# Kernel optimization log

Hardware: AMD Instinct MI355X
Metric: run time of the kernel (lower is better)

The kernel has to match this reference:

```python
import jax, jax.numpy as jnp
import numpy as np

B, S, CTX, DIM = 2, 2048, 2048, 2048
H, HKV, HD = 16, 4, 128
HID = 5464  # 4*ceil(int(4*DIM*2/3)/4)
EPS = 1.1920929e-07  # torch eps=None -> finfo(fp32).eps
REP = H // HKV


def rmsnorm(x, w):
    return x * jax.lax.rsqrt(jnp.mean(x * x, axis=-1, keepdims=True) + EPS) * w


def rotate_half(x):
    # interleaved rotate: out[::2] = -x[1::2], out[1::2] = x[::2]
    x2 = x.reshape(x.shape[:-1] + (-1, 2))
    return jnp.stack([-x2[..., 1], x2[..., 0]], axis=-1).reshape(x.shape)


def masked_attn(q, k, v, mask):
    # q,k,v: [B,H,Sq/Sk,D]; mask broadcastable to [B,H,Sq,Sk]
    scale = 1.0 / jnp.sqrt(jnp.asarray(q.shape[-1], q.dtype))
    s = jnp.einsum('bhqd,bhkd->bhqk', q, k) * scale
    s = jnp.where(mask, s, jnp.asarray(-1e30, s.dtype))
    p = jax.nn.softmax(s, axis=-1)
    p = jnp.where(mask, p, 0.0)  # fully-masked rows -> 0 output (flex_attention semantics)
    return jnp.einsum('bhqk,bhkd->bhqd', p, v)


def setup_inputs() -> dict:
    key = jax.random.key(0)
    ks = jax.random.split(key, 20)
    std = 0.02
    return {
        'x': jax.random.normal(ks[0], (B, S, DIM), jnp.float32),
        'context': jax.random.normal(ks[1], (B, CTX, DIM), jnp.float32),
        'freqs_cos': jax.random.uniform(ks[2], (S, 1, HD), jnp.float32),
        'freqs_sin': jax.random.uniform(ks[3], (S, 1, HD), jnp.float32),
        'wqkv': jax.random.normal(ks[4], ((H + 2 * HKV) * HD, DIM), jnp.float32) * std,
        'wo_self': jax.random.normal(ks[5], (DIM, DIM), jnp.float32) * std,
        'qn_self': jnp.ones((HD,), jnp.float32),
        'kn_self': jnp.ones((HD,), jnp.float32),
        'wq': jax.random.normal(ks[6], (H * HD, DIM), jnp.float32) * std,
        'wkv': jax.random.normal(ks[7], (2 * HKV * HD, DIM), jnp.float32) * std,
        'wo_cross': jax.random.normal(ks[8], (DIM, DIM), jnp.float32) * std,
        'qn_cross': jnp.ones((HD,), jnp.float32),
        'kn_cross': jnp.ones((HD,), jnp.float32),
        'w1': jax.random.normal(ks[9], (HID, DIM), jnp.float32) * std,
        'w2': jax.random.normal(ks[10], (DIM, HID), jnp.float32) * std,
        'attn_norm_w': jnp.ones((DIM,), jnp.float32),
        'cross_norm_w': jnp.ones((DIM,), jnp.float32),
        'ffn_norm_w': jnp.ones((DIM,), jnp.float32),
        'vis_mask': jax.random.randint(ks[11], (B, S), 0, 2).astype(bool),
        'context_mask': jax.random.randint(ks[12], (B, CTX), 0, 2).astype(bool),
    }


def reference(x, context, freqs_cos, freqs_sin, wqkv, wo_self, qn_self, kn_self,
              wq, wkv, wo_cross, qn_cross, kn_cross, w1, w2,
              attn_norm_w, cross_norm_w, ffn_norm_w, vis_mask, context_mask):
    b, s, _ = x.shape
    ctx = context.shape[1]

    # ---- self-attention (prenorm) ----
    h0 = rmsnorm(x, attn_norm_w)
    qkv = h0 @ wqkv.T
    xq = qkv[..., :H * HD].reshape(b, s, H, HD)
    xk = qkv[..., H * HD:(H + HKV) * HD].reshape(b, s, HKV, HD)
    xv = qkv[..., (H + HKV) * HD:].reshape(b, s, HKV, HD)
    xq = rmsnorm(xq, qn_self)   # qk-norm BEFORE rope in self-attn
    xk = rmsnorm(xk, kn_self)
    xq = xq * freqs_cos + rotate_half(xq) * freqs_sin
    xk = xk * freqs_cos + rotate_half(xk) * freqs_sin
    q = xq.transpose(0, 2, 1, 3)
    k = jnp.repeat(xk.transpose(0, 2, 1, 3), REP, axis=1)
    v = jnp.repeat(xv.transpose(0, 2, 1, 3), REP, axis=1)
    m_self = vis_mask[:, None, :, None] & vis_mask[:, None, None, :]
    a = masked_attn(q, k, v, m_self)
    h = x + a.transpose(0, 2, 1, 3).reshape(b, s, DIM) @ wo_self.T

    # ---- cross-attention (prenorm) ----
    hc = rmsnorm(h, cross_norm_w)
    xq = (hc @ wq.T).reshape(b, s, H, HD)
    kv = context @ wkv.T
    xk = kv[..., :HKV * HD].reshape(b, ctx, HKV, HD)
    xv = kv[..., HKV * HD:].reshape(b, ctx, HKV, HD)
    xq = xq * freqs_cos + rotate_half(xq) * freqs_sin  # rope on q BEFORE qk-norm in cross-attn
    xq = rmsnorm(xq, qn_cross)
    xk = rmsnorm(xk, kn_cross)
    q = xq.transpose(0, 2, 1, 3)
    k = jnp.repeat(xk.transpose(0, 2, 1, 3), REP, axis=1)
    v = jnp.repeat(xv.transpose(0, 2, 1, 3), REP, axis=1)
    m_cross = context_mask[:, None, None, :]
    a = masked_attn(q, k, v, m_cross)
    h = h + a.transpose(0, 2, 1, 3).reshape(b, s, DIM) @ wo_cross.T

    # ---- FFN (silu) ----
    hf = rmsnorm(h, ffn_norm_w)
    return h + jax.nn.silu(hf @ w1.T) @ w2.T
```

## Files before the change

### kernel.cpp

```cpp
#include <hip/hip_runtime.h>

#define DEVI __device__ __forceinline__

typedef __attribute__((ext_vector_type(4))) float f32x4;
typedef __attribute__((ext_vector_type(8))) __bf16 bf16x8;

static constexpr float EPS = 1.1920929e-07f;

DEVI float bf2f(unsigned short u){ return __uint_as_float(((unsigned)u)<<16); }
DEVI unsigned short f2bfu(float f){
  unsigned u = __float_as_uint(f);
  u += 0x7fffu + ((u>>16)&1u);
  return (unsigned short)(u>>16);
}
DEVI unsigned pack2(float a, float b){ return (unsigned)f2bfu(a) | ((unsigned)f2bfu(b)<<16); }

DEVI void gload16(const void* g, const void* l){
  __builtin_amdgcn_global_load_lds((const __attribute__((address_space(1))) void*)g,
                                   (__attribute__((address_space(3))) void*)l, 16, 0, 0);
}

__global__ void k_masknorm(const unsigned* __restrict__ vin, const unsigned* __restrict__ cin,
                           unsigned char* __restrict__ vout, unsigned char* __restrict__ cout){
  __shared__ int smode;
  const int t = threadIdx.x;
  if (t==0) smode = 0;
  __syncthreads();
  unsigned loc = 0;
  for (int i=t; i<1024; i+=256) loc |= (vin[i] > 1u);
  if (loc) smode = 1;
  __syncthreads();
  if (smode){
    for (int i=t; i<1024; i+=256){
      ((unsigned*)vout)[i] = vin[i];
      ((unsigned*)cout)[i] = cin[i];
    }
  } else {
    const int* vi = (const int*)vin; const int* ci = (const int*)cin;
    for (int i=t; i<4096; i+=256){
      vout[i] = (unsigned char)(vi[i] != 0);
      cout[i] = (unsigned char)(ci[i] != 0);
    }
  }
}

__global__ void k_conv(const float* __restrict__ s, unsigned short* __restrict__ d, int n4){
  int i = blockIdx.x*256 + threadIdx.x;
  if (i >= n4) return;
  float4 v = ((const float4*)s)[i];
  uint2 u; u.x = pack2(v.x, v.y); u.y = pack2(v.z, v.w);
  ((uint2*)d)[i] = u;
}
__global__ void k_convpad_rows(const float* __restrict__ s, unsigned short* __restrict__ d,
                               int R, int C, int Rp){
  int i = blockIdx.x*256 + threadIdx.x;
  int total = (Rp*C)>>2;
  if (i >= total) return;
  uint2 u; u.x = 0u; u.y = 0u;
  if (i*4 < R*C){ float4 v = ((const float4*)s)[i]; u.x = pack2(v.x,v.y); u.y = pack2(v.z,v.w); }
  ((uint2*)d)[i] = u;
}
__global__ void k_convpad_cols(const float* __restrict__ s, unsigned short* __restrict__ d,
                               int N, int K, int Kp){
  int i = blockIdx.x*256 + threadIdx.x;
  int total = (N*Kp)>>2;
  if (i >= total) return;
  int i4 = i*4; int n = i4/Kp; int k = i4 - n*Kp;
  uint2 u; u.x = 0u; u.y = 0u;
  if (k < K){ float4 v = *(const float4*)(s + (size_t)n*K + k); u.x = pack2(v.x,v.y); u.y = pack2(v.z,v.w); }
  ((uint2*)d)[i] = u;
}

__global__ void k_rms(const float* __restrict__ X, const float* __restrict__ W,
                      unsigned short* __restrict__ Y){
  const int row = blockIdx.x, tid = threadIdx.x;
  const float* x = X + (size_t)row*2048;
  float4 v0 = ((const float4*)x)[tid*2];
  float4 v1 = ((const float4*)x)[tid*2+1];
  float ss = v0.x*v0.x+v0.y*v0.y+v0.z*v0.z+v0.w*v0.w
           + v1.x*v1.x+v1.y*v1.y+v1.z*v1.z+v1.w*v1.w;
  #pragma unroll
  for (int o=32;o;o>>=1) ss += __shfl_xor(ss, o);
  __shared__ float red[4];
  if ((tid&63)==0) red[tid>>6] = ss;
  __syncthreads();
  float tot = red[0]+red[1]+red[2]+red[3];
  float rs = rsqrtf(tot*(1.0f/2048.0f) + EPS);
  float4 w0 = ((const float4*)W)[tid*2];
  float4 w1 = ((const float4*)W)[tid*2+1];
  uint4 u;
  u.x = pack2(v0.x*rs*w0.x, v0.y*rs*w0.y);
  u.y = pack2(v0.z*rs*w0.z, v0.w*rs*w0.w);
  u.z = pack2(v1.x*rs*w1.x, v1.y*rs*w1.y);
  u.w = pack2(v1.z*rs*w1.z, v1.w*rs*w1.w);
  *(uint4*)(Y + (size_t)row*2048 + tid*8) = u;
}

template<int EPI>
__global__ void k_gemm(const unsigned short* __restrict__ A, const unsigned short* __restrict__ Bw,
                       void* Cout, const float* resid, int M, int N, int K){
  __shared__ __align__(16) unsigned short sm[16384];
  const int tid = threadIdx.x;
  const int w = tid>>6, l = tid&63, g = l>>4, q = l&15;
  const int bm = blockIdx.y<<7, bn = blockIdx.x<<7;
  const int wr = (w>>1)<<6, wc = (w&1)<<6;
  f32x4 acc[4][4];
  #pragma unroll
  for (int a=0;a<4;++a)
    #pragma unroll
    for (int b2=0;b2<4;++b2) acc[a][b2] = f32x4{0.f,0.f,0.f,0.f};

  const unsigned short* Ag = A + (size_t)bm*K;
  const unsigned short* Bg = Bw + (size_t)bn*K;
  const int nk = K>>5;
  int cur = 0;

  auto STAGE = [&](int buf, int kt){
    #pragma unroll
    for (int i=0;i<2;++i){
      int L = (i*256+tid)*16;
      int r = L>>6; int ce = (L&63)>>1;
      int lofs = __builtin_amdgcn_readfirstlane(buf*8192 + i*4096 + (tid>>6)*1024);
      gload16(Ag + (size_t)r*K + (kt<<5) + ce, (const char*)sm + lofs);
    }
    #pragma unroll
    for (int i=0;i<2;++i){
      int L = (i*256+tid)*16;
      int r = L>>6; int ce = (L&63)>>1;
      int lofs = __builtin_amdgcn_readfirstlane(16384 + buf*8192 + i*4096 + (tid>>6)*1024);
      gload16(Bg + (size_t)r*K + (kt<<5) + ce, (const char*)sm + lofs);
    }
  };

  STAGE(0, 0);
  __syncthreads();
  for (int kt=0; kt<nk; ++kt){
    if (kt+1 < nk) STAGE(cur^1, kt+1);
    const unsigned short* Ab = sm + cur*4096;
    const unsigned short* Bb = sm + 8192 + cur*4096;
    bf16x8 af[4], bfr[4];
    #pragma unroll
    for (int mi=0;mi<4;++mi) af[mi] = *(const bf16x8*)(Ab + (wr + mi*16 + q)*32 + g*8);
    #pragma unroll
    for (int ni=0;ni<4;++ni) bfr[ni] = *(const bf16x8*)(Bb + (wc + ni*16 + q)*32 + g*8);
    #pragma unroll
    for (int mi=0;mi<4;++mi)
      #pragma unroll
      for (int ni=0;ni<4;++ni)
        acc[mi][ni] = __builtin_amdgcn_mfma_f32_16x16x32_bf16(af[mi], bfr[ni], acc[mi][ni], 0,0,0);
    __syncthreads();
    cur ^= 1;
  }
  #pragma unroll
  for (int mi=0;mi<4;++mi)
    #pragma unroll
    for (int ni=0;ni<4;++ni)
      #pragma unroll
      for (int r=0;r<4;++r){
        int row = bm + wr + mi*16 + g*4 + r;
        int col = bn + wc + ni*16 + q;
        size_t idx = (size_t)row*N + col;
        float v = acc[mi][ni][r];
        if (EPI==0) ((unsigned short*)Cout)[idx] = f2bfu(v);
        else if (EPI==1){ float sg = v/(1.0f+__expf(-v)); ((unsigned short*)Cout)[idx] = f2bfu(sg); }
        else ((float*)Cout)[idx] = resid[idx] + v;
      }
}

__global__ void k_self_pp(const unsigned short* __restrict__ qkv, const float* __restrict__ fc,
                          const float* __restrict__ fs, const float* __restrict__ qn,
                          const float* __restrict__ kn,
                          unsigned short* __restrict__ Qb, unsigned short* __restrict__ Kb,
                          unsigned short* __restrict__ Vt){
  const int row = blockIdx.x;
  const int b = row>>11, s = row&2047;
  const int w = threadIdx.x>>6, l = threadIdx.x&63;
  const int d0 = 2*l, d1 = d0+1;
  const float c0 = fc[s*128+d0], c1 = fc[s*128+d1];
  const float s0 = fs[s*128+d0], s1 = fs[s*128+d1];
  #pragma unroll
  for (int it=0; it<6; ++it){
    const int hh = it*4 + w;
    const unsigned short* src = qkv + (size_t)row*3072 + hh*128;
    if (hh >= 20){
      const int hv = hh - 20;
      size_t base = ((size_t)(b*4 + hv))*128*2048;
      Vt[base + (size_t)d0*2048 + s] = src[d0];
      Vt[base + (size_t)d1*2048 + s] = src[d1];
    } else {
      float x0 = bf2f(src[d0]), x1 = bf2f(src[d1]);
      float ss = x0*x0 + x1*x1;
      #pragma unroll
      for (int o=32;o;o>>=1) ss += __shfl_xor(ss, o);
      float rs = rsqrtf(ss*(1.0f/128.0f) + EPS);
      if (hh < 16){
        float y0 = x0*rs*qn[d0], y1 = x1*rs*qn[d1];
        *(unsigned*)(Qb + (((size_t)(b*16 + hh)*2048 + s)*128) + d0)
          = pack2(y0*c0 - y1*s0, y1*c1 + y0*s1);
      } else {
        float y0 = x0*rs*kn[d0], y1 = x1*rs*kn[d1];
        *(unsigned*)(Kb + (((size_t)(b*4 + (hh-16))*2048 + s)*128) + d0)
          = pack2(y0*c0 - y1*s0, y1*c1 + y0*s1);
      }
    }
  }
}

__global__ void k_crossq_pp(const unsigned short* __restrict__ qc, const float* __restrict__ fc,
                            const float* __restrict__ fs, const float* __restrict__ qn,
                            unsigned short* __restrict__ Qb){
  const int row = blockIdx.x;
  const int b = row>>11, s = row&2047;
  const int w = threadIdx.x>>6, l = threadIdx.x&63;
  const int d0 = 2*l, d1 = d0+1;
  const float c0 = fc[s*128+d0], c1 = fc[s*128+d1];
  const float s0 = fs[s*128+d0], s1 = fs[s*128+d1];
  #pragma unroll
  for (int it=0; it<4; ++it){
    const int hh = it*4 + w;
    const unsigned short* src = qc + (size_t)row*2048 + hh*128;
    float x0 = bf2f(src[d0]), x1 = bf2f(src[d1]);
    float y0 = x0*c0 - x1*s0;
    float y1 = x1*c1 + x0*s1;
    float ss = y0*y0 + y1*y1;
    #pragma unroll
    for (int o=32;o;o>>=1) ss += __shfl_xor(ss, o);
    float rs = rsqrtf(ss*(1.0f/128.0f) + EPS);
    *(unsigned*)(Qb + (((size_t)(b*16 + hh)*2048 + s)*128) + d0)
      = pack2(y0*rs*qn[d0], y1*rs*qn[d1]);
  }
}

__global__ void k_crosskv_pp(const unsigned short* __restrict__ kvc, const float* __restrict__ kn,
                             unsigned short* __restrict__ Kb, unsigned short* __restrict__ Vt){
  const int row = blockIdx.x;
  const int b = row>>11, s = row&2047;
  const int w = threadIdx.x>>6, l = threadIdx.x&63;
  const int d0 = 2*l, d1 = d0+1;
  #pragma unroll
  for (int it=0; it<2; ++it){
    const int hh = it*4 + w;
    const unsigned short* src = kvc + (size_t)row*1024 + hh*128;
    if (hh < 4){
      float x0 = bf2f(src[d0]), x1 = bf2f(src[d1]);
      float ss = x0*x0 + x1*x1;
      #pragma unroll
      for (int o=32;o;o>>=1) ss += __shfl_xor(ss, o);
      float rs = rsqrtf(ss*(1.0f/128.0f) + EPS);
      *(unsigned*)(Kb + (((size_t)(b*4 + hh)*2048 + s)*128) + d0)
        = pack2(x0*rs*kn[d0], x1*rs*kn[d1]);
    } else {
      const int hv = hh-4;
      size_t base = ((size_t)(b*4 + hv))*128*2048;
      Vt[base + (size_t)d0*2048 + s] = src[d0];
      Vt[base + (size_t)d1*2048 + s] = src[d1];
    }
  }
}

template<bool QMASK>
__global__ void k_attn(const unsigned short* __restrict__ Qg, const unsigned short* __restrict__ Kg,
                       const unsigned short* __restrict__ Vtg,
                       const unsigned char* __restrict__ qm, const unsigned char* __restrict__ km,
                       unsigned short* __restrict__ Og, int H, int HKV){
  constexpr int SK = 2048, SQ = 2048, NT = SK/64;
  constexpr float SCALE = 0.08838834764831845f;
  __shared__ __align__(16) char smem[75776];
  const int qt = blockIdx.x, h = blockIdx.y, b = blockIdx.z;
  const int hk = h / (H/HKV);
  const int tid = threadIdx.x, w = tid>>6, l = tid&63, g = l>>4, q = l&15;

  {
    const unsigned long long* mp = (const unsigned long long*)(km + (size_t)b*SK);
    ((unsigned long long*)(smem + 73728))[tid] = mp[tid];
  }

  const size_t qrow = (size_t)(b*H + h)*SQ + qt*64 + w*16 + q;
  bf16x8 qf[4];
  #pragma unroll
  for (int ks=0;ks<4;++ks) qf[ks] = *(const bf16x8*)(Qg + qrow*128 + ks*32 + g*8);

  f32x4 oacc[8];
  #pragma unroll
  for (int i=0;i<8;++i) oacc[i] = f32x4{0.f,0.f,0.f,0.f};
  float m_run = -1e30f, l_run = 0.f;

  const unsigned short* Kt0 = Kg + (size_t)(b*HKV + hk)*SK*128;
  const unsigned short* Vt0 = Vtg + (size_t)(b*HKV + hk)*128*SK;
  const unsigned char* mlds = (const unsigned char*)(smem + 73728);
  char* Pl = smem + 65536 + w*2048;

  auto STAGE_T = [&](int t, int p){
    #pragma unroll
    for (int i=0;i<4;++i){
      int L = (i*256+tid)*16;
      int r = L>>8, c16 = (L>>4)&15;
      int c = (c16 & 8) | ((c16 & 7) ^ (r & 7));
      int lofs = __builtin_amdgcn_readfirstlane(p*16384 + i*4096 + w*1024);
      gload16(Kt0 + (size_t)(t*64 + r)*128 + c*8, smem + lofs);
    }
    #pragma unroll
    for (int i=0;i<4;++i){
      int L = (i*256+tid)*16;
      int d = L>>7, c8 = (L>>4)&7;
      int c = c8 ^ (d & 7);
      int lofs = __builtin_amdgcn_readfirstlane(32768 + p*16384 + i*4096 + w*1024);
      gload16(Vt0 + (size_t)d*SK + t*64 + c*8, smem + lofs);
    }
  };

  STAGE_T(0, 0);

  for (int t=0; t<NT; ++t){
    const int p = t&1;
    asm volatile("s_waitcnt lgkmcnt(0)" ::: "memory");
    __builtin_amdgcn_s_barrier();
    asm volatile("" ::: "memory");
    if (t+1 < NT){
      STAGE_T(t+1, p^1);
      asm volatile("s_waitcnt vmcnt(8)" ::: "memory");
    } else {
      asm volatile("s_waitcnt vmcnt(0)" ::: "memory");
    }
    __builtin_amdgcn_s_barrier();
    asm volatile("" ::: "memory");

    const char* Kb_ = smem + p*16384;
    const char* Vb_ = smem + 32768 + p*16384;

    f32x4 sacc[4];
    #pragma unroll
    for (int i=0;i<4;++i) sacc[i] = f32x4{0.f,0.f,0.f,0.f};
    __builtin_amdgcn_s_setprio(1);
    #pragma unroll
    for (int ks=0;ks<4;++ks){
      #pragma unroll
      for (int mi=0;mi<4;++mi){
        int kcol = mi*16 + q;
        int c = 4*ks + g;
        int c16 = (c & 8) | ((c & 7) ^ (kcol & 7));
        bf16x8 ak = *(const bf16x8*)(Kb_ + kcol*256 + c16*16);
        sacc[mi] = __builtin_amdgcn_mfma_f32_16x16x32_bf16(ak, qf[ks], sacc[mi], 0,0,0);
      }
    }
    __builtin_amdgcn_s_setprio(0);
    float sv[4][4];
    float mloc = -1e30f;
    #pragma unroll
    for (int mi=0;mi<4;++mi)
      #pragma unroll
      for (int r=0;r<4;++r){
        int kidx = t*64 + mi*16 + g*4 + r;
        float v = mlds[kidx] ? sacc[mi][r]*SCALE : -1e30f;
        sv[mi][r] = v;
        mloc = fmaxf(mloc, v);
      }
    mloc = fmaxf(mloc, __shfl_xor(mloc, 16));
    mloc = fmaxf(mloc, __shfl_xor(mloc, 32));
    float mnew = fmaxf(m_run, mloc);
    float alpha = __expf(m_run - mnew);
    float rsum = 0.f;
    unsigned pb[4][2];
    #pragma unroll
    for (int mi=0;mi<4;++mi){
      float p0 = (sv[mi][0] > -5e29f) ? __expf(sv[mi][0] - mnew) : 0.f;
      float p1 = (sv[mi][1] > -5e29f) ? __expf(sv[mi][1] - mnew) : 0.f;
      float p2 = (sv[mi][2] > -5e29f) ? __expf(sv[mi][2] - mnew) : 0.f;
      float p3 = (sv[mi][3] > -5e29f) ? __expf(sv[mi][3] - mnew) : 0.f;
      float q0 = bf2f(f2bfu(p0)), q1 = bf2f(f2bfu(p1));
      float q2 = bf2f(f2bfu(p2)), q3 = bf2f(f2bfu(p3));
      rsum += (q0+q1)+(q2+q3);
      pb[mi][0] = pack2(q0, q1);
      pb[mi][1] = pack2(q2, q3);
    }
    rsum += __shfl_xor(rsum, 16);
    rsum += __shfl_xor(rsum, 32);
    l_run = l_run*alpha + rsum;
    m_run = mnew;
    #pragma unroll
    for (int i=0;i<8;++i) oacc[i] *= alpha;

    #pragma unroll
    for (int mi=0;mi<4;++mi){
      int c16 = (2*mi + (g>>1)) ^ (q & 7);
      uint2 uu; uu.x = pb[mi][0]; uu.y = pb[mi][1];
      *(uint2*)(Pl + q*128 + c16*16 + (g&1)*8) = uu;
    }
    asm volatile("" ::: "memory");

    __builtin_amdgcn_s_setprio(1);
    #pragma unroll
    for (int ks=0;ks<2;++ks){
      int c16 = (4*ks + g) ^ (q & 7);
      bf16x8 pf = *(const bf16x8*)(Pl + q*128 + c16*16);
      #pragma unroll
      for (int mi=0;mi<8;++mi){
        int d = mi*16 + q;
        bf16x8 vf = *(const bf16x8*)(Vb_ + d*128 + c16*16);
        oacc[mi] = __builtin_amdgcn_mfma_f32_16x16x32_bf16(vf, pf, oacc[mi], 0,0,0);
      }
    }
    __builtin_amdgcn_s_setprio(0);
  }

  float inv = (l_run > 0.f) ? 1.0f/l_run : 0.f;
  if (QMASK){
    if (!qm[(size_t)b*SQ + qt*64 + w*16 + q]) inv = 0.f;
  }
  __syncthreads();
  float* Ot = (float*)smem;
  #pragma unroll
  for (int mi=0;mi<8;++mi)
    #pragma unroll
    for (int r=0;r<4;++r){
      int d = mi*16 + g*4 + r;
      Ot[d*65 + w*16 + q] = oacc[mi][r]*inv;
    }
  __syncthreads();
  int qloc = tid>>2, seg = tid&3;
  int srow = qt*64 + qloc;
  size_t obase = ((size_t)b*SQ + srow)*(size_t)(H*128) + (size_t)h*128 + seg*32;
  #pragma unroll
  for (int p4=0;p4<4;++p4){
    float vv[8];
    #pragma unroll
    for (int j=0;j<8;++j) vv[j] = Ot[(seg*32 + p4*8 + j)*65 + qloc];
    uint4 u;
    u.x = pack2(vv[0],vv[1]); u.y = pack2(vv[2],vv[3]);
    u.z = pack2(vv[4],vv[5]); u.w = pack2(vv[6],vv[7]);
    *(uint4*)(Og + obase + p4*8) = u;
  }
}

extern "C" void kernel_launch(void* const* d_in, const int* in_sizes, int n_in,
                              void* d_out, int out_size, void* d_ws, size_t ws_size,
                              hipStream_t stream){
  const float* x        = (const float*)d_in[0];
  const float* ctx      = (const float*)d_in[1];
  const float* fc       = (const float*)d_in[2];
  const float* fs       = (const float*)d_in[3];
  const float* wqkv     = (const float*)d_in[4];
  const float* wo_self  = (const float*)d_in[5];
  const float* qn_self  = (const float*)d_in[6];
  const float* kn_self  = (const float*)d_in[7];
  const float* wq       = (const float*)d_in[8];
  const float* wkv      = (const float*)d_in[9];
  const float* wo_cross = (const float*)d_in[10];
  const float* qn_cross = (const float*)d_in[11];
  const float* kn_cross = (const float*)d_in[12];
  const float* w1       = (const float*)d_in[13];
  const float* w2       = (const float*)d_in[14];
  const float* attn_nw  = (const float*)d_in[15];
  const float* cross_nw = (const float*)d_in[16];
  const float* ffn_nw   = (const float*)d_in[17];
  const unsigned* vis_raw   = (const unsigned*)d_in[18];
  const unsigned* cmask_raw = (const unsigned*)d_in[19];
  float* out = (float*)d_out;

  char* ws = (char*)d_ws;
  unsigned short* wslot = (unsigned short*)(ws);
  unsigned short* ctxbf = (unsigned short*)(ws +  22544384);
  unsigned short* nbuf  = (unsigned short*)(ws +  39321600);
  unsigned short* qkvb  = (unsigned short*)(ws +  56098816);
  unsigned short* Qb    = (unsigned short*)(ws +  81264640);
  unsigned short* Kb    = (unsigned short*)(ws +  98041856);
  unsigned short* Vtb   = (unsigned short*)(ws + 102236160);
  unsigned short* aob   = (unsigned short*)(ws + 106430464);
  unsigned short* midb  = (unsigned short*)(ws + 123207680);
  unsigned char*  visN  = (unsigned char*)(ws + 168296448);
  unsigned char*  cmkN  = (unsigned char*)(ws + 168300544);
  unsigned short* qcb   = qkvb;
  unsigned short* kvcb  = qkvb + 8388608;

  auto conv = [&](const float* s, unsigned short* dst, size_t n){
    int n4 = (int)(n>>2);
    k_conv<<<(n4+255)/256, 256, 0, stream>>>(s, dst, n4);
  };

  k_masknorm<<<1,256,0,stream>>>(vis_raw, cmask_raw, visN, cmkN);

  conv(ctx, ctxbf, (size_t)4096*2048);
  k_rms<<<4096,256,0,stream>>>(x, attn_nw, nbuf);
  conv(wqkv, wslot, (size_t)3072*2048);
  k_gemm<0><<<dim3(24,32),256,0,stream>>>(nbuf, wslot, qkvb, nullptr, 4096,3072,2048);
  k_self_pp<<<4096,256,0,stream>>>(qkvb, fc, fs, qn_self, kn_self, Qb, Kb, Vtb);
  k_attn<true><<<dim3(32,16,2),256,0,stream>>>(Qb, Kb, Vtb, visN, visN, aob, 16, 4);
  conv(wo_self, wslot, (size_t)2048*2048);
  k_gemm<2><<<dim3(16,32),256,0,stream>>>(aob, wslot, out, x, 4096,2048,2048);

  k_rms<<<4096,256,0,stream>>>(out, cross_nw, nbuf);
  conv(wq, wslot, (size_t)2048*2048);
  k_gemm<0><<<dim3(16,32),256,0,stream>>>(nbuf, wslot, qcb, nullptr, 4096,2048,2048);
  conv(wkv, wslot, (size_t)1024*2048);
  k_gemm<0><<<dim3(8,32),256,0,stream>>>(ctxbf, wslot, kvcb, nullptr, 4096,1024,2048);
  k_crossq_pp<<<4096,256,0,stream>>>(qcb, fc, fs, qn_cross, Qb);
  k_crosskv_pp<<<4096,256,0,stream>>>(kvcb, kn_cross, Kb, Vtb);
  k_attn<false><<<dim3(32,16,2),256,0,stream>>>(Qb, Kb, Vtb, nullptr, cmkN, aob, 16, 4);
  conv(wo_cross, wslot, (size_t)2048*2048);
  k_gemm<2><<<dim3(16,32),256,0,stream>>>(aob, wslot, out, out, 4096,2048,2048);

  k_rms<<<4096,256,0,stream>>>(out, ffn_nw, nbuf);
  k_convpad_rows<<<(5504*2048/4+255)/256,256,0,stream>>>(w1, wslot, 5464, 2048, 5504);
  k_gemm<1><<<dim3(43,32),256,0,stream>>>(nbuf, wslot, midb, nullptr, 4096,5504,2048);
  k_convpad_cols<<<(2048*5504/4+255)/256,256,0,stream>>>(w2, wslot, 2048, 5464, 5504);
  k_gemm<2><<<dim3(16,32),256,0,stream>>>(midb, wslot, out, out, 4096,2048,5504);

  (void)in_sizes; (void)n_in; (void)out_size; (void)ws_size;
}
```

Baseline: 942.2 us.

## Fold softmax scale into Q, use exp2, additive mask bias, lazy rescale

Pre-multiplies Q by scale*log2(e) in the preprocessing kernels so attention can use raw v_exp_f32 (exp2) without a per-score multiply. The byte mask is expanded once into an additive float bias in LDS, replacing per-element select branches. The running-max rescale of the output accumulators is skipped unless the max grows by more than a threshold, and P is packed with the hardware bf16 convert instruction. Risks: the row sum now uses unrounded probabilities while PV uses bf16 values, and fully-masked rows or lazy rescaling could change numerics slightly.

```diff
diff --git a/kernel.cpp b/kernel.cpp
--- a/kernel.cpp
+++ b/kernel.cpp
@@ -6,6 +6,7 @@
 typedef __attribute__((ext_vector_type(8))) __bf16 bf16x8;
 
 static constexpr float EPS = 1.1920929e-07f;
+static constexpr float SC2L = 0.12751551960234575f;
 
 DEVI float bf2f(unsigned short u){ return __uint_as_float(((unsigned)u)<<16); }
 DEVI unsigned short f2bfu(float f){
@@ -14,6 +15,10 @@
   return (unsigned short)(u>>16);
 }
 DEVI unsigned pack2(float a, float b){ return (unsigned)f2bfu(a) | ((unsigned)f2bfu(b)<<16); }
+DEVI float exp2a(float x){ float r; asm("v_exp_f32 %0, %1" : "=v"(r) : "v"(x)); return r; }
+DEVI unsigned cvtpk(float lo, float hi){
+  unsigned r; asm("v_cvt_pk_bf16_f32 %0, %1, %2" : "=v"(r) : "v"(lo), "v"(hi)); return r;
+}
 
 DEVI void gload16(const void* g, const void* l){
   __builtin_amdgcn_global_load_lds((const __attribute__((address_space(1))) void*)g,
@@ -196,7 +201,7 @@
       if (hh < 16){
         float y0 = x0*rs*qn[d0], y1 = x1*rs*qn[d1];
         *(unsigned*)(Qb + (((size_t)(b*16 + hh)*2048 + s)*128) + d0)
-          = pack2(y0*c0 - y1*s0, y1*c1 + y0*s1);
+          = pack2((y0*c0 - y1*s0)*SC2L, (y1*c1 + y0*s1)*SC2L);
       } else {
         float y0 = x0*rs*kn[d0], y1 = x1*rs*kn[d1];
         *(unsigned*)(Kb + (((size_t)(b*4 + (hh-16))*2048 + s)*128) + d0)
@@ -227,7 +232,7 @@
     for (int o=32;o;o>>=1) ss += __shfl_xor(ss, o);
     float rs = rsqrtf(ss*(1.0f/128.0f) + EPS);
     *(unsigned*)(Qb + (((size_t)(b*16 + hh)*2048 + s)*128) + d0)
-      = pack2(y0*rs*qn[d0], y1*rs*qn[d1]);
+      = pack2(y0*rs*qn[d0]*SC2L, y1*rs*qn[d1]*SC2L);
   }
 }
 
@@ -264,15 +269,17 @@
                        const unsigned char* __restrict__ qm, const unsigned char* __restrict__ km,
                        unsigned short* __restrict__ Og, int H, int HKV){
   constexpr int SK = 2048, SQ = 2048, NT = SK/64;
-  constexpr float SCALE = 0.08838834764831845f;
-  __shared__ __align__(16) char smem[75776];
+  __shared__ __align__(16) char smem[81920];
   const int qt = blockIdx.x, h = blockIdx.y, b = blockIdx.z;
   const int hk = h / (H/HKV);
   const int tid = threadIdx.x, w = tid>>6, l = tid&63, g = l>>4, q = l&15;
 
   {
-    const unsigned long long* mp = (const unsigned long long*)(km + (size_t)b*SK);
-    ((unsigned long long*)(smem + 73728))[tid] = mp[tid];
+    const unsigned long long mv = ((const unsigned long long*)(km + (size_t)b*SK))[tid];
+    float* bl = (float*)(smem + 73728);
+    #pragma unroll
+    for (int j=0;j<8;++j)
+      bl[tid*8+j] = ((mv>>(8*j)) & 0xffull) ? 0.0f : -3.0e38f;
   }
 
   const size_t qrow = (size_t)(b*H + h)*SQ + qt*64 + w*16 + q;
@@ -283,11 +290,11 @@
   f32x4 oacc[8];
   #pragma unroll
   for (int i=0;i<8;++i) oacc[i] = f32x4{0.f,0.f,0.f,0.f};
-  float m_run = -1e30f, l_run = 0.f;
+  float m_run = -1.0e30f, l_run = 0.f;
 
   const unsigned short* Kt0 = Kg + (size_t)(b*HKV + hk)*SK*128;
   const unsigned short* Vt0 = Vtg + (size_t)(b*HKV + hk)*128*SK;
-  const unsigned char* mlds = (const unsigned char*)(smem + 73728);
+  const float* biasf = (const float*)(smem + 73728);
   char* Pl = smem + 65536 + w*2048;
 
   auto STAGE_T = [&](int t, int p){
@@ -344,41 +351,44 @@
       }
     }
     __builtin_amdgcn_s_setprio(0);
+
     float sv[4][4];
-    float mloc = -1e30f;
-    #pragma unroll
-    for (int mi=0;mi<4;++mi)
+    float mloc = -3.0e38f;
+    #pragma unroll
+    for (int mi=0;mi<4;++mi){
+      f32x4 bb = *(const f32x4*)(biasf + t*64 + mi*16 + g*4);
       #pragma unroll
       for (int r=0;r<4;++r){
-        int kidx = t*64 + mi*16 + g*4 + r;
-        float v = mlds[kidx] ? sacc[mi][r]*SCALE : -1e30f;
+        float v = sacc[mi][r] + bb[r];
         sv[mi][r] = v;
         mloc = fmaxf(mloc, v);
       }
+    }
     mloc = fmaxf(mloc, __shfl_xor(mloc, 16));
     mloc = fmaxf(mloc, __shfl_xor(mloc, 32));
-    float mnew = fmaxf(m_run, mloc);
-    float alpha = __expf(m_run - mnew);
+    if (!__all(mloc - m_run <= 8.0f)){
+      float mnew = fmaxf(m_run, mloc);
+      float alpha = exp2a(m_run - mnew);
+      l_run *= alpha;
+      #pragma unroll
+      for (int i=0;i<8;++i) oacc[i] *= alpha;
+      m_run = mnew;
+    }
     float rsum = 0.f;
     unsigned pb[4][2];
     #pragma unroll
     for (int mi=0;mi<4;++mi){
-      float p0 = (sv[mi][0] > -5e29f) ? __expf(sv[mi][0] - mnew) : 0.f;
-      float p1 = (sv[mi][1] > -5e29f) ? __expf(sv[mi][1] - mnew) : 0.f;
-      float p2 = (sv[mi][2] > -5e29f) ? __expf(sv[mi][2] - mnew) : 0.f;
-      float p3 = (sv[mi][3] > -5e29f) ? __expf(sv[mi][3] - mnew) : 0.f;
-      float q0 = bf2f(f2bfu(p0)), q1 = bf2f(f2bfu(p1));
-      float q2 = bf2f(f2bfu(p2)), q3 = bf2f(f2bfu(p3));
-      rsum += (q0+q1)+(q2+q3);
-      pb[mi][0] = pack2(q0, q1);
-      pb[mi][1] = pack2(q2, q3);
+      float p0 = exp2a(sv[mi][0] - m_run);
+      float p1 = exp2a(sv[mi][1] - m_run);
+      float p2 = exp2a(sv[mi][2] - m_run);
+      float p3 = exp2a(sv[mi][3] - m_run);
+      rsum += (p0+p1)+(p2+p3);
+      pb[mi][0] = cvtpk(p0, p1);
+      pb[mi][1] = cvtpk(p2, p3);
     }
     rsum += __shfl_xor(rsum, 16);
     rsum += __shfl_xor(rsum, 32);
-    l_run = l_run*alpha + rsum;
-    m_run = mnew;
-    #pragma unroll
-    for (int i=0;i<8;++i) oacc[i] *= alpha;
+    l_run += rsum;
 
     #pragma unroll
     for (int mi=0;mi<4;++mi){
```

After: 906.4 us. 3.8% less time.
